# Optimization experiments

Hardware: AMD Instinct MI355X
Metric: run time of the kernel (lower is better)

## Reference

```python
import jax, jax.numpy as jnp
import numpy as np

D_MODEL = 1024
NHEAD = 16
HEAD_DIM = D_MODEL // NHEAD
LN_EPS = 1e-5


def setup_inputs() -> dict:
    key = jax.random.key(0)
    ks = jax.random.split(key, 6)
    B, S = 4, 4096
    x = jax.random.normal(ks[0], (B, S, D_MODEL), dtype=jnp.float32)
    scale = 0.02
    Wq = jax.random.normal(ks[1], (D_MODEL, D_MODEL), dtype=jnp.float32) * scale
    Wv = jax.random.normal(ks[2], (D_MODEL, D_MODEL), dtype=jnp.float32) * scale
    Wo = jax.random.normal(ks[3], (D_MODEL, D_MODEL), dtype=jnp.float32) * scale
    Wg = jax.random.normal(ks[4], (D_MODEL, D_MODEL), dtype=jnp.float32) * scale
    beta = jnp.full((NHEAD,), -0.2, dtype=jnp.float32)
    ln_gamma = jnp.ones((D_MODEL,), dtype=jnp.float32)
    ln_beta = jnp.zeros((D_MODEL,), dtype=jnp.float32)
    return {"x": x, "Wq": Wq, "Wv": Wv, "Wo": Wo, "Wg": Wg,
            "beta": beta, "ln_gamma": ln_gamma, "ln_beta": ln_beta}


def _ema_scan(lam, v):
    # v: [B, S, H, D]; lam: [1, 1, H, 1]
    # s_t = lam * s_{t-1} + v_t, computed with a parallel associative scan
    # on pairs (a, b) representing the affine map s -> a*s + b.
    a = jnp.broadcast_to(lam, v.shape)

    def combine(e1, e2):
        a1, b1 = e1
        a2, b2 = e2
        return a1 * a2, a2 * b1 + b2

    _, state = jax.lax.associative_scan(combine, (a, v), axis=1)
    return state


def reference(x, Wq, Wv, Wo, Wg, beta, ln_gamma, ln_beta):
    B, S, _ = x.shape
    q = (x @ Wq.T).reshape(B, S, NHEAD, HEAD_DIM)
    v = (x @ Wv.T).reshape(B, S, NHEAD, HEAD_DIM)
    lam = jax.nn.sigmoid(beta).reshape(1, 1, NHEAD, 1).astype(v.dtype)
    state = _ema_scan(lam, v)                      # [B, S, H, D]
    y = (q * state).reshape(B, S, D_MODEL)
    # LayerNorm over last dim
    mu = jnp.mean(y, axis=-1, keepdims=True)
    var = jnp.mean(jnp.square(y - mu), axis=-1, keepdims=True)
    y = (y - mu) * jax.lax.rsqrt(var + LN_EPS) * ln_gamma + ln_beta
    gate = jax.nn.silu(x @ Wg.T)
    y = y * gate
    return y @ Wo.T
```

## Files before the change

kernel.cpp:

```cpp
#include <hip/hip_runtime.h>

#define D_MODEL 1024
#define NHEAD 16
#define LN_EPS 1e-5f
#define CHUNK 64
#define S_LEN 4096

typedef unsigned short u16;
typedef __attribute__((ext_vector_type(8))) short short8;
typedef __attribute__((ext_vector_type(4))) float f32x4;

__device__ __forceinline__ u16 f2b(float f) {
  unsigned u = __builtin_bit_cast(unsigned, f);
  u += 0x7FFFu + ((u >> 16) & 1u);
  return (u16)(u >> 16);
}
__device__ __forceinline__ float b2f(u16 s) {
  return __builtin_bit_cast(float, ((unsigned)s) << 16);
}

__global__ __launch_bounds__(256) void cvt_f32_bf16(const float4* __restrict__ src,
                                                    ushort4* __restrict__ dst, int n4) {
  int i = blockIdx.x * blockDim.x + threadIdx.x;
  int stride = gridDim.x * blockDim.x;
  for (; i < n4; i += stride) {
    float4 f = src[i];
    ushort4 o;
    o.x = f2b(f.x); o.y = f2b(f.y); o.z = f2b(f.z); o.w = f2b(f.w);
    dst[i] = o;
  }
}

__global__ void lam_kernel(const float* __restrict__ beta, float* __restrict__ lam) {
  int h = threadIdx.x;
  if (h < NHEAD) lam[h] = 1.f / (1.f + __expf(-beta[h]));
}


__device__ __forceinline__ void glds16(const u16* g, const u16* l) {
  __builtin_amdgcn_global_load_lds(
      (const __attribute__((address_space(1))) unsigned*)g,
      (__attribute__((address_space(3))) unsigned*)l, 16, 0, 0);
}

#define BAR() asm volatile("s_barrier" ::: "memory")

template <typename OutT>
__global__ __launch_bounds__(512, 2) void gemm256(const u16* __restrict__ X,
                                                  const u16* __restrict__ W,
                                                  OutT* __restrict__ Out,
                                                  int M, int N, int K) {
  __shared__ u16 sm[8][8192];
  const int tid = threadIdx.x;
  const int lane = tid & 63;
  const int wave = tid >> 6;
  const int ln15 = lane & 15, lh = lane >> 4;
  const int wr = wave >> 2, wc = wave & 3;
  const int bm = blockIdx.x * 256, bn = blockIdx.y * 256;
  const int NT = K >> 6;

  const int srow = tid >> 3;
  const int scol = ((tid & 7) ^ (srow & 7)) << 3;
  const u16* Asrc = X + (size_t)(bm + srow) * K + scol;
  const u16* Bsrc = W + (size_t)(bn + srow) * K + scol;
  const int ldsw = wave * 512;

#define STAGE(u, h, tile, src)                                          \
  { const u16* _g = (src) + (size_t)((h) * 128) * K + (tile) * 64;      \
    glds16(_g,                 &sm[u][ldsw]);                           \
    glds16(_g + (size_t)64 * K, &sm[u][ldsw + 4096]); }

  const char* smb = (const char*)&sm[0][0];
  const char* Ard = smb + wr * 16384 + ln15 * 128;
  const char* Brd = smb + (2 + (wc >> 1)) * 16384 + ((wc & 1) * 64 + ln15) * 128;
  const int swz0 = ((lh ^ (ln15 & 7)) << 4);
  const int swz1 = (((4 + lh) ^ (ln15 & 7)) << 4);

  f32x4 acc[8][4];
  f32x4 zero = {0.f, 0.f, 0.f, 0.f};
  #pragma unroll
  for (int m = 0; m < 8; ++m)
    #pragma unroll
    for (int n = 0; n < 4; ++n) acc[m][n] = zero;

  STAGE(0, 0, 0, Asrc); STAGE(1, 1, 0, Asrc);
  STAGE(2, 0, 0, Bsrc); STAGE(3, 1, 0, Bsrc);
  STAGE(4, 0, 1, Asrc); STAGE(5, 1, 1, Asrc);
  asm volatile("s_waitcnt vmcnt(4)" ::: "memory");
  BAR();

  for (int t = 0; t < NT; ++t) {
    const int d = t & 1;
    const int db = d * 65536;
    const int od = (d ^ 1) * 4;
    const int sd = d * 4;
    short8 a[8][2], b[4][2];

    #pragma unroll
    for (int m = 0; m < 4; ++m) {
      a[m][0] = *(const short8*)(Ard + db + m * 2048 + swz0);
      a[m][1] = *(const short8*)(Ard + db + m * 2048 + swz1);
    }
    #pragma unroll
    for (int n = 0; n < 2; ++n) {
      b[n][0] = *(const short8*)(Brd + db + n * 2048 + swz0);
      b[n][1] = *(const short8*)(Brd + db + n * 2048 + swz1);
    }
    if (t + 1 < NT) STAGE(od + 2, 0, t + 1, Bsrc);
    BAR();
    asm volatile("s_waitcnt lgkmcnt(0)" ::: "memory");
    __builtin_amdgcn_sched_barrier(0);
    __builtin_amdgcn_s_setprio(1);
    #pragma unroll
    for (int m = 0; m < 4; ++m)
      #pragma unroll
      for (int n = 0; n < 2; ++n) {
        acc[m][n] = __builtin_amdgcn_mfma_f32_16x16x32_bf16(a[m][0], b[n][0], acc[m][n], 0, 0, 0);
        acc[m][n] = __builtin_amdgcn_mfma_f32_16x16x32_bf16(a[m][1], b[n][1], acc[m][n], 0, 0, 0);
      }
    __builtin_amdgcn_s_setprio(0);
    __builtin_amdgcn_sched_barrier(0);
    BAR();

    #pragma unroll
    for (int m = 4; m < 8; ++m) {
      a[m][0] = *(const short8*)(Ard + db + m * 2048 + swz0);
      a[m][1] = *(const short8*)(Ard + db + m * 2048 + swz1);
    }
    if (t + 1 < NT) STAGE(od + 3, 1, t + 1, Bsrc);
    BAR();
    asm volatile("s_waitcnt lgkmcnt(0)" ::: "memory");
    __builtin_amdgcn_sched_barrier(0);
    __builtin_amdgcn_s_setprio(1);
    #pragma unroll
    for (int m = 4; m < 8; ++m)
      #pragma unroll
      for (int n = 0; n < 2; ++n) {
        acc[m][n] = __builtin_amdgcn_mfma_f32_16x16x32_bf16(a[m][0], b[n][0], acc[m][n], 0, 0, 0);
        acc[m][n] = __builtin_amdgcn_mfma_f32_16x16x32_bf16(a[m][1], b[n][1], acc[m][n], 0, 0, 0);
      }
    __builtin_amdgcn_s_setprio(0);
    __builtin_amdgcn_sched_barrier(0);
    BAR();

    #pragma unroll
    for (int n = 2; n < 4; ++n) {
      b[n][0] = *(const short8*)(Brd + db + n * 2048 + swz0);
      b[n][1] = *(const short8*)(Brd + db + n * 2048 + swz1);
    }
    if (t + 2 < NT) STAGE(sd + 0, 0, t + 2, Asrc);
    BAR();
    asm volatile("s_waitcnt lgkmcnt(0)" ::: "memory");
    __builtin_amdgcn_sched_barrier(0);
    __builtin_amdgcn_s_setprio(1);
    #pragma unroll
    for (int m = 0; m < 4; ++m)
      #pragma unroll
      for (int n = 2; n < 4; ++n) {
        acc[m][n] = __builtin_amdgcn_mfma_f32_16x16x32_bf16(a[m][0], b[n][0], acc[m][n], 0, 0, 0);
        acc[m][n] = __builtin_amdgcn_mfma_f32_16x16x32_bf16(a[m][1], b[n][1], acc[m][n], 0, 0, 0);
      }
    __builtin_amdgcn_s_setprio(0);
    __builtin_amdgcn_sched_barrier(0);
    BAR();

    if (t + 2 < NT) STAGE(sd + 1, 1, t + 2, Asrc);
    __builtin_amdgcn_sched_barrier(0);
    __builtin_amdgcn_s_setprio(1);
    #pragma unroll
    for (int m = 4; m < 8; ++m)
      #pragma unroll
      for (int n = 2; n < 4; ++n) {
        acc[m][n] = __builtin_amdgcn_mfma_f32_16x16x32_bf16(a[m][0], b[n][0], acc[m][n], 0, 0, 0);
        acc[m][n] = __builtin_amdgcn_mfma_f32_16x16x32_bf16(a[m][1], b[n][1], acc[m][n], 0, 0, 0);
      }
    __builtin_amdgcn_s_setprio(0);
    __builtin_amdgcn_sched_barrier(0);
    if (t + 2 < NT) {
      asm volatile("s_waitcnt vmcnt(4)" ::: "memory");
    } else if (t + 1 < NT) {
      asm volatile("s_waitcnt vmcnt(0)" ::: "memory");
    }
    BAR();
  }
#undef STAGE

  #pragma unroll
  for (int m = 0; m < 8; ++m)
    #pragma unroll
    for (int n = 0; n < 4; ++n)
      #pragma unroll
      for (int r = 0; r < 4; ++r) {
        int row = bm + wr * 128 + m * 16 + lh * 4 + r;
        int col = bn + wc * 64 + n * 16 + ln15;
        float vv = acc[m][n][r];
        if constexpr (sizeof(OutT) == 2) Out[(size_t)row * N + col] = f2b(vv);
        else                             Out[(size_t)row * N + col] = vv;
      }
}

__global__ __launch_bounds__(256) void scan_local(u16* __restrict__ v,
                                                  float* __restrict__ carry,
                                                  const float* __restrict__ lam,
                                                  int S, int nch, int ld) {
  int bj = blockIdx.x;
  int b = bj / nch, j = bj - b * nch;
  int col0 = threadIdx.x * 4;
  float l = lam[col0 >> 6];
  float s0 = 0.f, s1 = 0.f, s2 = 0.f, s3 = 0.f;
  size_t base = ((size_t)b * S + (size_t)j * CHUNK) * ld + col0;
  for (int t = 0; t < CHUNK; ++t) {
    ushort4* p = (ushort4*)(v + base + (size_t)t * ld);
    ushort4 u = *p;
    s0 = l * s0 + b2f(u.x);
    s1 = l * s1 + b2f(u.y);
    s2 = l * s2 + b2f(u.z);
    s3 = l * s3 + b2f(u.w);
    u.x = f2b(s0); u.y = f2b(s1); u.z = f2b(s2); u.w = f2b(s3);
    *p = u;
  }
  size_t cb = (size_t)bj * D_MODEL + col0;
  carry[cb] = s0; carry[cb + 1] = s1; carry[cb + 2] = s2; carry[cb + 3] = s3;
}

__global__ void scan_carry(float* __restrict__ carry, const float* __restrict__ lam,
                           int B, int nch) {
  int idx = blockIdx.x * blockDim.x + threadIdx.x;
  if (idx >= B * D_MODEL) return;
  int b = idx >> 10, col = idx & (D_MODEL - 1);
  float l = lam[col >> 6];
  float lC = __powf(l, (float)CHUNK);
  float c = 0.f;
  for (int j = 0; j < nch; ++j) {
    size_t a = ((size_t)(b * nch + j)) * D_MODEL + col;
    c = lC * c + carry[a];
    carry[a] = c;
  }
}

__global__ __launch_bounds__(256) void ew_ln(const u16* __restrict__ qvg,
    const float* __restrict__ carry, const float* __restrict__ lam,
    const float* __restrict__ gamma, const float* __restrict__ lbeta,
    u16* __restrict__ yout, int S, int nch, int ld) {
  int row = blockIdx.x;
  int b = row / S, s = row - b * S;
  int j = s / CHUNK, tl = s - j * CHUNK;
  int tid = threadIdx.x;
  int col0 = tid * 4;
  size_t rb = (size_t)row * ld;

  ushort4 qu = *(const ushort4*)(qvg + rb + col0);
  ushort4 su = *(const ushort4*)(qvg + rb + D_MODEL + col0);
  float st[4] = {b2f(su.x), b2f(su.y), b2f(su.z), b2f(su.w)};
  if (j > 0) {
    float l = lam[col0 >> 6];
    float p = __powf(l, (float)(tl + 1));
    const float4 c4 = *(const float4*)(carry + ((size_t)(b * nch + j - 1)) * D_MODEL + col0);
    st[0] += p * c4.x; st[1] += p * c4.y; st[2] += p * c4.z; st[3] += p * c4.w;
  }
  float q[4] = {b2f(qu.x), b2f(qu.y), b2f(qu.z), b2f(qu.w)};
  float y[4];
  float sum = 0.f, sumsq = 0.f;
  #pragma unroll
  for (int i = 0; i < 4; ++i) {
    y[i] = q[i] * st[i];
    sum += y[i];
    sumsq += y[i] * y[i];
  }
  #pragma unroll
  for (int off = 32; off > 0; off >>= 1) {
    sum += __shfl_down(sum, off);
    sumsq += __shfl_down(sumsq, off);
  }
  __shared__ float red[8];
  int ln = tid & 63, wv = tid >> 6;
  if (ln == 0) { red[wv] = sum; red[4 + wv] = sumsq; }
  __syncthreads();
  sum = red[0] + red[1] + red[2] + red[3];
  sumsq = red[4] + red[5] + red[6] + red[7];
  float mu = sum * (1.f / 1024.f);
  float var = sumsq * (1.f / 1024.f) - mu * mu;
  float rstd = rsqrtf(var + LN_EPS);

  float4 gm = *(const float4*)(gamma + col0);
  float4 bt = *(const float4*)(lbeta + col0);
  ushort4 gu = *(const ushort4*)(qvg + rb + 2 * D_MODEL + col0);
  float gv[4]  = {b2f(gu.x), b2f(gu.y), b2f(gu.z), b2f(gu.w)};
  float gmv[4] = {gm.x, gm.y, gm.z, gm.w};
  float btv[4] = {bt.x, bt.y, bt.z, bt.w};
  u16 ov[4];
  #pragma unroll
  for (int i = 0; i < 4; ++i) {
    float gate = gv[i] / (1.f + __expf(-gv[i]));
    float oo = ((y[i] - mu) * rstd * gmv[i] + btv[i]) * gate;
    ov[i] = f2b(oo);
  }
  ushort4 o; o.x = ov[0]; o.y = ov[1]; o.z = ov[2]; o.w = ov[3];
  *(ushort4*)(yout + (size_t)row * D_MODEL + col0) = o;
}

extern "C" void kernel_launch(void* const* d_in, const int* in_sizes, int n_in,
                              void* d_out, int out_size, void* d_ws, size_t ws_size,
                              hipStream_t stream) {
  const float* x     = (const float*)d_in[0];
  const float* Wq    = (const float*)d_in[1];
  const float* Wv    = (const float*)d_in[2];
  const float* Wo    = (const float*)d_in[3];
  const float* Wg    = (const float*)d_in[4];
  const float* beta  = (const float*)d_in[5];
  const float* gamma = (const float*)d_in[6];
  const float* lbeta = (const float*)d_in[7];
  float* out = (float*)d_out;

  const int BS = in_sizes[0] / D_MODEL;
  const int S = S_LEN;
  const int B = BS / S;
  const int nch = S / CHUNK;
  const size_t nx = (size_t)BS * D_MODEL;
  const size_t nw = (size_t)D_MODEL * D_MODEL;
  const int N3 = 3 * D_MODEL;

  char* w = (char*)d_ws;
  u16* xb   = (u16*)w;  w += nx * 2;
  u16* wqvg = (u16*)w;  w += 3 * nw * 2;
  u16* wob  = (u16*)w;  w += nw * 2;
  u16* qvg  = (u16*)w;  w += (size_t)BS * N3 * 2;
  u16* yb   = (u16*)w;  w += nx * 2;
  float* carry = (float*)w;  w += (size_t)B * nch * D_MODEL * 4;
  float* lam = (float*)w;

  cvt_f32_bf16<<<2048, 256, 0, stream>>>((const float4*)x,  (ushort4*)xb, (int)(nx / 4));
  cvt_f32_bf16<<<1024, 256, 0, stream>>>((const float4*)Wq, (ushort4*)(wqvg), (int)(nw / 4));
  cvt_f32_bf16<<<1024, 256, 0, stream>>>((const float4*)Wv, (ushort4*)(wqvg + nw), (int)(nw / 4));
  cvt_f32_bf16<<<1024, 256, 0, stream>>>((const float4*)Wg, (ushort4*)(wqvg + 2 * nw), (int)(nw / 4));
  cvt_f32_bf16<<<1024, 256, 0, stream>>>((const float4*)Wo, (ushort4*)wob, (int)(nw / 4));
  lam_kernel<<<1, 64, 0, stream>>>(beta, lam);

  dim3 g1(BS / 256, N3 / 256);
  gemm256<u16><<<g1, 512, 0, stream>>>(xb, wqvg, qvg, BS, N3, D_MODEL);

  scan_local<<<B * nch, 256, 0, stream>>>(qvg + D_MODEL, carry, lam, S, nch, N3);
  scan_carry<<<(B * D_MODEL + 255) / 256, 256, 0, stream>>>(carry, lam, B, nch);
  ew_ln<<<BS, 256, 0, stream>>>(qvg, carry, lam, gamma, lbeta, yb, S, nch, N3);

  dim3 g2(BS / 256, D_MODEL / 256);
  gemm256<float><<<g2, 512, 0, stream>>>(yb, wob, out, BS, D_MODEL, D_MODEL);
}
```

Before: 259.2 us.

## Software-pipeline LDS fragment reads across GEMM k-tiles and cut barriers

```diff
diff --git a/kernel.cpp b/kernel.cpp
--- a/kernel.cpp
+++ b/kernel.cpp
@@ -44,6 +44,7 @@
 }
 
 #define BAR() asm volatile("s_barrier" ::: "memory")
+#define SB0() __builtin_amdgcn_sched_barrier(0)
 
 template <typename OutT>
 __global__ __launch_bounds__(512, 2) void gemm256(const u16* __restrict__ X,
@@ -67,7 +68,7 @@
 
 #define STAGE(u, h, tile, src)                                          \
   { const u16* _g = (src) + (size_t)((h) * 128) * K + (tile) * 64;      \
-    glds16(_g,                 &sm[u][ldsw]);                           \
+    glds16(_g,                  &sm[u][ldsw]);                          \
     glds16(_g + (size_t)64 * K, &sm[u][ldsw + 4096]); }
 
   const char* smb = (const char*)&sm[0][0];
@@ -76,114 +77,80 @@
   const int swz0 = ((lh ^ (ln15 & 7)) << 4);
   const int swz1 = (((4 + lh) ^ (ln15 & 7)) << 4);
 
+#define RD_A(DB, MM, S) (*(const short8*)(Ard + (DB) + (MM) * 2048 + (S)))
+#define RD_B(DB, NN, S) (*(const short8*)(Brd + (DB) + (NN) * 2048 + (S)))
+
   f32x4 acc[8][4];
   f32x4 zero = {0.f, 0.f, 0.f, 0.f};
   #pragma unroll
   for (int m = 0; m < 8; ++m)
     #pragma unroll
     for (int n = 0; n < 4; ++n) acc[m][n] = zero;
+
+  short8 a[8][2], b[4][2];
+
+#define MFMA_Q(M0, N0)                                                        \
+  SB0();                                                                      \
+  __builtin_amdgcn_s_setprio(1);                                              \
+  _Pragma("unroll")                                                           \
+  for (int m = (M0); m < (M0) + 4; ++m)                                       \
+    _Pragma("unroll")                                                         \
+    for (int n = (N0); n < (N0) + 2; ++n) {                                   \
+      acc[m][n] = __builtin_amdgcn_mfma_f32_16x16x32_bf16(a[m][0], b[n][0], acc[m][n], 0, 0, 0); \
+      acc[m][n] = __builtin_amdgcn_mfma_f32_16x16x32_bf16(a[m][1], b[n][1], acc[m][n], 0, 0, 0); \
+    }                                                                         \
+  __builtin_amdgcn_s_setprio(0);                                              \
+  SB0();
 
   STAGE(0, 0, 0, Asrc); STAGE(1, 1, 0, Asrc);
   STAGE(2, 0, 0, Bsrc); STAGE(3, 1, 0, Bsrc);
   STAGE(4, 0, 1, Asrc); STAGE(5, 1, 1, Asrc);
   asm volatile("s_waitcnt vmcnt(4)" ::: "memory");
   BAR();
+  #pragma unroll
+  for (int m = 0; m < 4; ++m) { a[m][0] = RD_A(0, m, swz0); a[m][1] = RD_A(0, m, swz1); }
+  #pragma unroll
+  for (int n = 0; n < 4; ++n) { b[n][0] = RD_B(0, n, swz0); b[n][1] = RD_B(0, n, swz1); }
 
   for (int t = 0; t < NT; ++t) {
     const int d = t & 1;
     const int db = d * 65536;
+    const int odb = (d ^ 1) * 65536;
     const int od = (d ^ 1) * 4;
     const int sd = d * 4;
-    short8 a[8][2], b[4][2];
+    const int tB = (t + 1 < NT) ? t + 1 : NT - 1;
+    const int tA = (t + 2 < NT) ? t + 2 : NT - 1;
+
+    a[4][0] = RD_A(db, 4, swz0); a[4][1] = RD_A(db, 4, swz1);
+    a[5][0] = RD_A(db, 5, swz0); a[5][1] = RD_A(db, 5, swz1);
+    STAGE(od + 2, 0, tB, Bsrc);
+    MFMA_Q(0, 0)
+
+    a[6][0] = RD_A(db, 6, swz0); a[6][1] = RD_A(db, 6, swz1);
+    a[7][0] = RD_A(db, 7, swz0); a[7][1] = RD_A(db, 7, swz1);
+    STAGE(od + 3, 1, tB, Bsrc);
+    MFMA_Q(0, 2)
+    asm volatile("s_waitcnt vmcnt(4) lgkmcnt(0)" ::: "memory");
+    BAR();
 
     #pragma unroll
-    for (int m = 0; m < 4; ++m) {
-      a[m][0] = *(const short8*)(Ard + db + m * 2048 + swz0);
-      a[m][1] = *(const short8*)(Ard + db + m * 2048 + swz1);
-    }
-    #pragma unroll
-    for (int n = 0; n < 2; ++n) {
-      b[n][0] = *(const short8*)(Brd + db + n * 2048 + swz0);
-      b[n][1] = *(const short8*)(Brd + db + n * 2048 + swz1);
-    }
-    if (t + 1 < NT) STAGE(od + 2, 0, t + 1, Bsrc);
+    for (int m = 0; m < 4; ++m) { a[m][0] = RD_A(odb, m, swz0); a[m][1] = RD_A(odb, m, swz1); }
+    MFMA_Q(4, 2)
+    STAGE(sd + 0, 0, tA, Asrc);
+    asm volatile("s_waitcnt vmcnt(2)" ::: "memory");
     BAR();
-    asm volatile("s_waitcnt lgkmcnt(0)" ::: "memory");
-    __builtin_amdgcn_sched_barrier(0);
-    __builtin_amdgcn_s_setprio(1);
-    #pragma unroll
-    for (int m = 0; m < 4; ++m)
-      #pragma unroll
-      for (int n = 0; n < 2; ++n) {
-        acc[m][n] = __builtin_amdgcn_mfma_f32_16x16x32_bf16(a[m][0], b[n][0], acc[m][n], 0, 0, 0);
-        acc[m][n] = __builtin_amdgcn_mfma_f32_16x16x32_bf16(a[m][1], b[n][1], acc[m][n], 0, 0, 0);
-      }
-    __builtin_amdgcn_s_setprio(0);
-    __builtin_amdgcn_sched_barrier(0);
-    BAR();
-
-    #pragma unroll
-    for (int m = 4; m < 8; ++m) {
-      a[m][0] = *(const short8*)(Ard + db + m * 2048 + swz0);
-      a[m][1] = *(const short8*)(Ard + db + m * 2048 + swz1);
-    }
-    if (t + 1 < NT) STAGE(od + 3, 1, t + 1, Bsrc);
-    BAR();
-    asm volatile("s_waitcnt lgkmcnt(0)" ::: "memory");
-    __builtin_amdgcn_sched_barrier(0);
-    __builtin_amdgcn_s_setprio(1);
-    #pragma unroll
-    for (int m = 4; m < 8; ++m)
-      #pragma unroll
-      for (int n = 0; n < 2; ++n) {
-        acc[m][n] = __builtin_amdgcn_mfma_f32_16x16x32_bf16(a[m][0], b[n][0], acc[m][n], 0, 0, 0);
-        acc[m][n] = __builtin_amdgcn_mfma_f32_16x16x32_bf16(a[m][1], b[n][1], acc[m][n], 0, 0, 0);
-      }
-    __builtin_amdgcn_s_setprio(0);
-    __builtin_amdgcn_sched_barrier(0);
-    BAR();
-
-    #pragma unroll
-    for (int n = 2; n < 4; ++n) {
-      b[n][0] = *(const short8*)(Brd + db + n * 2048 + swz0);
-      b[n][1] = *(const short8*)(Brd + db + n * 2048 + swz1);
-    }
-    if (t + 2 < NT) STAGE(sd + 0, 0, t + 2, Asrc);
-    BAR();
-    asm volatile("s_waitcnt lgkmcnt(0)" ::: "memory");
-    __builtin_amdgcn_sched_barrier(0);
-    __builtin_amdgcn_s_setprio(1);
-    #pragma unroll
-    for (int m = 0; m < 4; ++m)
-      #pragma unroll
-      for (int n = 2; n < 4; ++n) {
-        acc[m][n] = __builtin_amdgcn_mfma_f32_16x16x32_bf16(a[m][0], b[n][0], acc[m][n], 0, 0, 0);
-        acc[m][n] = __builtin_amdgcn_mfma_f32_16x16x32_bf16(a[m][1], b[n][1], acc[m][n], 0, 0, 0);
-      }
-    __builtin_amdgcn_s_setprio(0);
-    __builtin_amdgcn_sched_barrier(0);
-    BAR();
-
-    if (t + 2 < NT) STAGE(sd + 1, 1, t + 2, Asrc);
-    __builtin_amdgcn_sched_barrier(0);
-    __builtin_amdgcn_s_setprio(1);
-    #pragma unroll
-    for (int m = 4; m < 8; ++m)
-      #pragma unroll
-      for (int n = 2; n < 4; ++n) {
-        acc[m][n] = __builtin_amdgcn_mfma_f32_16x16x32_bf16(a[m][0], b[n][0], acc[m][n], 0, 0, 0);
-        acc[m][n] = __builtin_amdgcn_mfma_f32_16x16x32_bf16(a[m][1], b[n][1], acc[m][n], 0, 0, 0);
-      }
-    __builtin_amdgcn_s_setprio(0);
-    __builtin_amdgcn_sched_barrier(0);
-    if (t + 2 < NT) {
-      asm volatile("s_waitcnt vmcnt(4)" ::: "memory");
-    } else if (t + 1 < NT) {
-      asm volatile("s_waitcnt vmcnt(0)" ::: "memory");
-    }
-    BAR();
+
+    b[2][0] = RD_B(odb, 2, swz0); b[2][1] = RD_B(odb, 2, swz1);
+    b[3][0] = RD_B(odb, 3, swz0); b[3][1] = RD_B(odb, 3, swz1);
+    MFMA_Q(4, 0)
+    b[0][0] = RD_B(odb, 0, swz0); b[0][1] = RD_B(odb, 0, swz1);
+    b[1][0] = RD_B(odb, 1, swz0); b[1][1] = RD_B(odb, 1, swz1);
+    STAGE(sd + 1, 1, tA, Asrc);
   }
 #undef STAGE
+#undef RD_A
+#undef RD_B
+#undef MFMA_Q
 
   #pragma unroll
   for (int m = 0; m < 8; ++m)
```

Result: faster. 252.5 us (-2.6%).
